# Performance work log

Hardware: AMD Instinct MI355X
Metric: run time of the kernel (lower is better)

## Reference

```python
import jax, jax.numpy as jnp
import numpy as np
from jax.ops import segment_sum, segment_max

N = 50000
E = 800000
F_IN = 128
F_HEAD = 32
HEADS = 8
N_CLASSES = 32
NEG_SLOPE = 0.2


def setup_inputs() -> dict:
    key = jax.random.key(0)
    ks = jax.random.split(key, 12)
    x = jax.random.normal(ks[0], (N, F_IN), dtype=jnp.float32)
    edge_index = jax.random.randint(ks[1], (2, E), 0, N, dtype=jnp.int64)
    # layer 1 params (in=128 -> heads=8, out=32)
    s1 = 1.0 / np.sqrt(F_IN)
    W1 = jax.random.uniform(ks[2], (F_IN, HEADS * F_HEAD), jnp.float32, -s1, s1)
    a_src1 = jax.random.uniform(ks[3], (HEADS, F_HEAD), jnp.float32, -s1, s1)
    a_dst1 = jax.random.uniform(ks[4], (HEADS, F_HEAD), jnp.float32, -s1, s1)
    b1 = jnp.zeros((HEADS * F_HEAD,), jnp.float32)
    # layer 2 params (in=256 -> heads=1, out=32)
    s2 = 1.0 / np.sqrt(HEADS * F_HEAD)
    W2 = jax.random.uniform(ks[5], (HEADS * F_HEAD, N_CLASSES), jnp.float32, -s2, s2)
    a_src2 = jax.random.uniform(ks[6], (1, N_CLASSES), jnp.float32, -s2, s2)
    a_dst2 = jax.random.uniform(ks[7], (1, N_CLASSES), jnp.float32, -s2, s2)
    b2 = jnp.zeros((N_CLASSES,), jnp.float32)
    return {"x": x, "edge_index": edge_index, "W1": W1, "a_src1": a_src1,
            "a_dst1": a_dst1, "b1": b1, "W2": W2, "a_src2": a_src2,
            "a_dst2": a_dst2, "b2": b2}


def gat_conv(x, W, a_src, a_dst, b, src, dst, heads, out_ch):
    n = x.shape[0]
    h = (x @ W).reshape(n, heads, out_ch)                  # [N,H,F]
    alpha_src = jnp.einsum('nhf,hf->nh', h, a_src)         # [N,H]
    alpha_dst = jnp.einsum('nhf,hf->nh', h, a_dst)
    e = alpha_src[src] + alpha_dst[dst]                    # [E,H]
    e = jnp.where(e > 0, e, NEG_SLOPE * e)                 # LeakyReLU(0.2)
    # segment softmax over edges grouped by destination node
    m = segment_max(e, dst, num_segments=n)                # [N,H]
    ex = jnp.exp(e - m[dst])
    denom = segment_sum(ex, dst, num_segments=n)           # [N,H]
    alpha = ex / (denom[dst] + 1e-16)                      # [E,H]
    out = segment_sum(alpha[:, :, None] * h[src], dst, num_segments=n)  # [N,H,F]
    return out.reshape(n, heads * out_ch) + b


def reference(x, edge_index, W1, a_src1, a_dst1, b1, W2, a_src2, a_dst2, b2):
    src, dst = edge_index[0], edge_index[1]
    h = gat_conv(x, W1, a_src1, a_dst1, b1, src, dst, HEADS, F_HEAD)
    h = jax.nn.elu(h)
    out = gat_conv(h, W2, a_src2, a_dst2, b2, src, dst, 1, N_CLASSES)
    return out
```

## Files before the change

kernel.cpp:

```cpp
#include <hip/hip_runtime.h>
#include <math.h>

#define NNODES 50000
#define NEDGES 800000
#define GB 782

typedef _Float16 f16;
typedef _Float16 f16x8 __attribute__((ext_vector_type(8)));
typedef _Float16 f16x4 __attribute__((ext_vector_type(4)));
typedef _Float16 f16x2 __attribute__((ext_vector_type(2)));
typedef float f32x4 __attribute__((ext_vector_type(4)));
typedef float f32x8 __attribute__((ext_vector_type(8)));
typedef unsigned short u16;


__global__ __launch_bounds__(256) void k_deg_wfrag(const int* __restrict__ ei, int* __restrict__ deg,
                                                   int* __restrict__ rank,
                                                   const float* __restrict__ W1, const float* __restrict__ W2,
                                                   f16* __restrict__ W1f, f16* __restrict__ W2f) {
    int bid = blockIdx.x;
    if (bid < NEDGES / 256) {
        int e = bid * 256 + threadIdx.x;
        rank[e] = atomicAdd(&deg[ei[NEDGES + e]], 1);
    } else {
        int id = (bid - NEDGES / 256) * 256 + threadIdx.x;
        if (id < 32768) {
            int k = id >> 8, c = id & 255;
            int kc = k >> 5, quad = (k & 31) >> 3, j = k & 7;
            W1f[(((kc << 8) + c) * 4 + quad) * 8 + j] = (f16)W1[id];
        } else {
            int i2 = id - 32768;
            int k = i2 >> 5, c = i2 & 31;
            int kc = k >> 5, quad = (k & 31) >> 3, j = k & 7;
            W2f[(((kc << 5) + c) * 4 + quad) * 8 + j] = (f16)W2[i2];
        }
    }
}

__global__ __launch_bounds__(256) void k_scanA(const int* __restrict__ deg, int* __restrict__ incl,
                                               int* __restrict__ partial) {
    int t = threadIdx.x;
    int i = blockIdx.x * 256 + t;
    int v = (i < NNODES) ? deg[i] : 0;
    int lane = t & 63, wid = t >> 6;
    int s = v;
#pragma unroll
    for (int d = 1; d < 64; d <<= 1) { int u = __shfl_up(s, d, 64); if (lane >= d) s += u; }
    __shared__ int wtot[4];
    if (lane == 63) wtot[wid] = s;
    __syncthreads();
    int off = 0;
    for (int w = 0; w < wid; ++w) off += wtot[w];
    s += off;
    if (i < NNODES) incl[i] = s;
    if (t == 255) partial[blockIdx.x] = s;
}

__global__ __launch_bounds__(256) void k_scanC(const int* __restrict__ deg, const int* __restrict__ incl,
                                               const int* __restrict__ partial, int* __restrict__ rowst) {
    int t = threadIdx.x, bid = blockIdx.x;
    int v = (t < bid) ? partial[t] : 0;
    int lane = t & 63, wid = t >> 6;
#pragma unroll
    for (int d = 1; d < 64; d <<= 1) v += __shfl_xor(v, d);
    __shared__ int ws[4];
    if (lane == 0) ws[wid] = v;
    __syncthreads();
    int choff = ws[0] + ws[1] + ws[2] + ws[3];
    int i = bid * 256 + t;
    if (i < NNODES) {
        int rs1 = incl[i] + choff;
        rowst[i + 1] = rs1;
        if (i == 0) rowst[0] = 0;
    }
}


__global__ __launch_bounds__(256) void k_gemm1_sc(const float* __restrict__ X, const f16* __restrict__ W1f,
                                                  const float* __restrict__ Asrc, const float* __restrict__ Adst,
                                                  f16* __restrict__ h1s, float* __restrict__ as1,
                                                  float* __restrict__ ad1, const int* __restrict__ ei,
                                                  const int* __restrict__ rowst, const int* __restrict__ rank,
                                                  u16* __restrict__ sd16) {
    __shared__ f16 sA[64 * 136];
    int bid = blockIdx.x;
    int t = threadIdx.x;
    if (bid >= GB) {
        int e = (bid - GB) * 256 + t;
        if (e < NEDGES) {
            int s = ei[e], d = ei[NEDGES + e];
            int pos = rowst[d] + rank[e];
            sd16[pos] = (u16)s;
        }
        return;
    }
    int bm = bid * 64;
    int lane = t & 63, w = t >> 6;
    int r = lane & 15, quad = lane >> 4;
    int cw = w * 64;
    f16x8 bf[4][4];
#pragma unroll
    for (int kc = 0; kc < 4; ++kc)
#pragma unroll
        for (int nt = 0; nt < 4; ++nt)
            bf[kc][nt] = *(const f16x8*)&W1f[(((kc << 8) + cw + nt * 16 + r) * 4 + quad) * 8];
#pragma unroll
    for (int i = 0; i < 8; ++i) {
        int idx = i * 256 + t;
        int row = idx >> 5, c4 = (idx & 31) << 2;
        int gr = bm + row;
        float4 v = make_float4(0.f, 0.f, 0.f, 0.f);
        if (gr < NNODES) v = *(const float4*)(X + (size_t)gr * 128 + c4);
        f16x4 h = {(f16)v.x, (f16)v.y, (f16)v.z, (f16)v.w};
        *(f16x4*)&sA[row * 136 + c4] = h;
    }
    __syncthreads();
    f32x4 acc[4][4];
#pragma unroll
    for (int rg = 0; rg < 4; ++rg)
#pragma unroll
        for (int nt = 0; nt < 4; ++nt) acc[rg][nt] = (f32x4){0.f, 0.f, 0.f, 0.f};
#pragma unroll
    for (int kc = 0; kc < 4; ++kc)
#pragma unroll
        for (int rg = 0; rg < 4; ++rg) {
            f16x8 a = *(f16x8*)&sA[(rg * 16 + r) * 136 + kc * 32 + quad * 8];
#pragma unroll
            for (int nt = 0; nt < 4; ++nt)
                acc[rg][nt] = __builtin_amdgcn_mfma_f32_16x16x32_f16(a, bf[kc][nt], acc[rg][nt], 0, 0, 0);
        }
#pragma unroll
    for (int rg = 0; rg < 4; ++rg)
#pragma unroll
        for (int nt = 0; nt < 4; ++nt)
#pragma unroll
            for (int i = 0; i < 4; ++i) {
                int gr = bm + rg * 16 + quad * 4 + i;
                if (gr < NNODES)
                    h1s[((size_t)(2 * w + (nt >> 1)) * NNODES + gr) * 32 + (nt & 1) * 16 + r] =
                        (f16)acc[rg][nt][i];
            }
    float asv[4], adv[4];
#pragma unroll
    for (int nt = 0; nt < 4; ++nt) {
        asv[nt] = Asrc[cw + nt * 16 + r];
        adv[nt] = Adst[cw + nt * 16 + r];
    }
#pragma unroll
    for (int rg = 0; rg < 4; ++rg)
#pragma unroll
        for (int i = 0; i < 4; ++i) {
            int gr = bm + rg * 16 + quad * 4 + i;
#pragma unroll
            for (int hh = 0; hh < 2; ++hh) {
                float ps = acc[rg][2 * hh][i] * asv[2 * hh] + acc[rg][2 * hh + 1][i] * asv[2 * hh + 1];
                float pd = acc[rg][2 * hh][i] * adv[2 * hh] + acc[rg][2 * hh + 1][i] * adv[2 * hh + 1];
#pragma unroll
                for (int off = 1; off < 16; off <<= 1) {
                    ps += __shfl_xor(ps, off);
                    pd += __shfl_xor(pd, off);
                }
                if (r == 0 && gr < NNODES) {
                    as1[(size_t)(2 * w + hh) * NNODES + gr] = ps;
                    ad1[(size_t)(2 * w + hh) * NNODES + gr] = pd;
                }
            }
        }
}

__global__ __launch_bounds__(256) void k_gemm2(const f16* __restrict__ h2s, const f16* __restrict__ W2f,
                                               const float* __restrict__ Asrc, const float* __restrict__ Adst,
                                               f16* __restrict__ gh, float* __restrict__ as2,
                                               float* __restrict__ ad2) {
    int t = threadIdx.x;
    int bm = blockIdx.x * 64;
    int lane = t & 63, w = t >> 6;
    int r = lane & 15, quad = lane >> 4;
    int r0 = w * 16;
    int gra = bm + r0 + r;
    int grac = gra < NNODES ? gra : 0;
    f32x4 acc[2];
    acc[0] = (f32x4){0.f, 0.f, 0.f, 0.f};
    acc[1] = (f32x4){0.f, 0.f, 0.f, 0.f};
#pragma unroll
    for (int kc = 0; kc < 8; ++kc) {
        f16x8 a = *(const f16x8*)(h2s + ((size_t)kc * NNODES + grac) * 32 + quad * 8);
#pragma unroll
        for (int nt = 0; nt < 2; ++nt) {
            f16x8 b = *(const f16x8*)&W2f[(((kc << 5) + nt * 16 + r) * 4 + quad) * 8];
            acc[nt] = __builtin_amdgcn_mfma_f32_16x16x32_f16(a, b, acc[nt], 0, 0, 0);
        }
    }
#pragma unroll
    for (int nt = 0; nt < 2; ++nt)
#pragma unroll
        for (int i = 0; i < 4; ++i) {
            int gr = bm + r0 + quad * 4 + i;
            if (gr < NNODES) gh[(size_t)gr * 32 + nt * 16 + r] = (f16)acc[nt][i];
        }
    float as0 = Asrc[r], as16 = Asrc[16 + r];
    float ad0 = Adst[r], ad16 = Adst[16 + r];
#pragma unroll
    for (int i = 0; i < 4; ++i) {
        int gr = bm + r0 + quad * 4 + i;
        float ps = acc[0][i] * as0 + acc[1][i] * as16;
        float pd = acc[0][i] * ad0 + acc[1][i] * ad16;
#pragma unroll
        for (int off = 1; off < 16; off <<= 1) {
            ps += __shfl_xor(ps, off);
            pd += __shfl_xor(pd, off);
        }
        if (r == 0 && gr < NNODES) { as2[gr] = ps; ad2[gr] = pd; }
    }
}

__global__ __launch_bounds__(256) void k_agg1(const int* __restrict__ rowst, const u16* __restrict__ sd16,
                                              const float* __restrict__ as1, const float* __restrict__ ad1,
                                              const f16* __restrict__ h1s, const float* __restrict__ b1,
                                              f16* __restrict__ h2s) {
    int bid = blockIdx.x;
    int sl = bid & 7;
    int ng = bid >> 3;
    int t = threadIdx.x;
    int w = t >> 6, lane = t & 63;
    int g = lane >> 2, cs = lane & 3;
    int c0 = cs << 3;
    int n = ng * 64 + w * 16 + g;
    if (n >= NNODES) return;
    int s = rowst[n], e = rowst[n + 1];
    float adn = ad1[(size_t)sl * NNODES + n];
    const f16* __restrict__ hp = h1s + (size_t)sl * NNODES * 32 + c0;
    const float* __restrict__ ap = as1 + (size_t)sl * NNODES;
    f32x8 acc = (f32x8){0.f, 0.f, 0.f, 0.f, 0.f, 0.f, 0.f, 0.f};
    float sum = 0.f;
    int j = s;
    for (; j + 7 < e; j += 8) {
        int si[8];
#pragma unroll
        for (int u = 0; u < 8; ++u) si[u] = (int)sd16[j + u];
        float xv[8];
#pragma unroll
        for (int u = 0; u < 8; ++u) xv[u] = ap[si[u]];
        f16x8 vv[8];
#pragma unroll
        for (int u = 0; u < 8; ++u) vv[u] = *(const f16x8*)(hp + (size_t)si[u] * 32);
        float ee[8];
#pragma unroll
        for (int u = 0; u < 8; ++u) {
            float x = xv[u] + adn;
            x = fmaxf(x, 0.2f * x);
            ee[u] = __expf(x);
            sum += ee[u];
        }
#pragma unroll
        for (int k = 0; k < 8; ++k) {
            float a = acc[k];
#pragma unroll
            for (int u = 0; u < 8; ++u) a += ee[u] * (float)vv[u][k];
            acc[k] = a;
        }
    }
    for (; j + 3 < e; j += 4) {
        int si[4];
#pragma unroll
        for (int u = 0; u < 4; ++u) si[u] = (int)sd16[j + u];
        float xv[4];
#pragma unroll
        for (int u = 0; u < 4; ++u) xv[u] = ap[si[u]];
        f16x8 vv[4];
#pragma unroll
        for (int u = 0; u < 4; ++u) vv[u] = *(const f16x8*)(hp + (size_t)si[u] * 32);
        float ee[4];
#pragma unroll
        for (int u = 0; u < 4; ++u) {
            float x = xv[u] + adn;
            x = fmaxf(x, 0.2f * x);
            ee[u] = __expf(x);
            sum += ee[u];
        }
#pragma unroll
        for (int k = 0; k < 8; ++k) {
            float a = acc[k];
#pragma unroll
            for (int u = 0; u < 4; ++u) a += ee[u] * (float)vv[u][k];
            acc[k] = a;
        }
    }
    for (; j < e; ++j) {
        int s0 = (int)sd16[j];
        float x0 = ap[s0] + adn;
        f16x8 v0 = *(const f16x8*)(hp + (size_t)s0 * 32);
        x0 = fmaxf(x0, 0.2f * x0);
        float e0 = __expf(x0);
        sum += e0;
#pragma unroll
        for (int k = 0; k < 8; ++k) acc[k] += e0 * (float)v0[k];
    }
    float inv = 1.f / (sum + 1e-16f);
    float4 b0 = *(const float4*)(b1 + sl * 32 + c0);
    float4 b4 = *(const float4*)(b1 + sl * 32 + c0 + 4);
    float o[8] = {acc[0] * inv + b0.x, acc[1] * inv + b0.y, acc[2] * inv + b0.z, acc[3] * inv + b0.w,
                  acc[4] * inv + b4.x, acc[5] * inv + b4.y, acc[6] * inv + b4.z, acc[7] * inv + b4.w};
    f16x8 oh;
#pragma unroll
    for (int k = 0; k < 8; ++k) {
        float v = o[k];
        v = v > 0.f ? v : __expf(v) - 1.f;
        oh[k] = (f16)v;
    }
    *(f16x8*)(h2s + ((size_t)sl * NNODES + n) * 32 + c0) = oh;
}

__global__ __launch_bounds__(256) void k_agg2(const int* __restrict__ rowst, const u16* __restrict__ sd16,
                                              const float* __restrict__ as2, const float* __restrict__ ad2,
                                              const f16* __restrict__ gh, const float* __restrict__ b2,
                                              float* __restrict__ out) {
    int w = threadIdx.x >> 6, lane = threadIdx.x & 63;
    int n = blockIdx.x * 4 + w;
    int s = rowst[n], e = rowst[n + 1];
    int slot = lane >> 4;
    int cp = lane & 15;
    float adn = ad2[n];
    const f16* __restrict__ gp = gh + 2 * cp;
    float a0 = 0.f, a1 = 0.f, sum = 0.f;
    int j = s + slot;
    for (; j + 12 < e; j += 16) {
        int si[4];
#pragma unroll
        for (int u = 0; u < 4; ++u) si[u] = (int)sd16[j + 4 * u];
        float xv[4];
#pragma unroll
        for (int u = 0; u < 4; ++u) xv[u] = as2[si[u]];
        f16x2 vv[4];
#pragma unroll
        for (int u = 0; u < 4; ++u) vv[u] = *(const f16x2*)(gp + (size_t)si[u] * 32);
        float ee[4];
#pragma unroll
        for (int u = 0; u < 4; ++u) {
            float x = xv[u] + adn;
            x = fmaxf(x, 0.2f * x);
            ee[u] = __expf(x);
            sum += ee[u];
        }
#pragma unroll
        for (int u = 0; u < 4; ++u) a0 += ee[u] * (float)vv[u][0];
#pragma unroll
        for (int u = 0; u < 4; ++u) a1 += ee[u] * (float)vv[u][1];
    }
    for (; j + 4 < e; j += 8) {
        int s0 = (int)sd16[j];
        int s1 = (int)sd16[j + 4];
        float x0 = as2[s0] + adn, x1 = as2[s1] + adn;
        f16x2 v0 = *(const f16x2*)(gp + (size_t)s0 * 32);
        f16x2 v1 = *(const f16x2*)(gp + (size_t)s1 * 32);
        x0 = fmaxf(x0, 0.2f * x0);
        x1 = fmaxf(x1, 0.2f * x1);
        float e0 = __expf(x0), e1 = __expf(x1);
        sum += e0 + e1;
        a0 += e0 * (float)v0[0] + e1 * (float)v1[0];
        a1 += e0 * (float)v0[1] + e1 * (float)v1[1];
    }
    for (; j < e; j += 4) {
        int s0 = (int)sd16[j];
        float x0 = as2[s0] + adn;
        f16x2 v0 = *(const f16x2*)(gp + (size_t)s0 * 32);
        x0 = fmaxf(x0, 0.2f * x0);
        float e0 = __expf(x0);
        sum += e0;
        a0 += e0 * (float)v0[0];
        a1 += e0 * (float)v0[1];
    }
#pragma unroll
    for (int d = 16; d < 64; d <<= 1) {
        sum += __shfl_xor(sum, d);
        a0 += __shfl_xor(a0, d);
        a1 += __shfl_xor(a1, d);
    }
    if (slot == 0) {
        float inv = 1.f / (sum + 1e-16f);
        float2 o;
        o.x = a0 * inv + b2[2 * cp];
        o.y = a1 * inv + b2[2 * cp + 1];
        *(float2*)(out + (size_t)n * 32 + 2 * cp) = o;
    }
}


extern "C" void kernel_launch(void* const* d_in, const int* in_sizes, int n_in,
                              void* d_out, int out_size, void* d_ws, size_t ws_size,
                              hipStream_t stream) {
    const float* x    = (const float*)d_in[0];
    const int*   ei   = (const int*)d_in[1];
    const float* W1   = (const float*)d_in[2];
    const float* As1  = (const float*)d_in[3];
    const float* Ad1  = (const float*)d_in[4];
    const float* b1   = (const float*)d_in[5];
    const float* W2   = (const float*)d_in[6];
    const float* As2  = (const float*)d_in[7];
    const float* Ad2  = (const float*)d_in[8];
    const float* b2   = (const float*)d_in[9];
    float* out = (float*)d_out;

    char* p = (char*)d_ws;
    auto alloc = [&](size_t bytes) -> char* {
        char* r = p;
        p += (bytes + 255) & ~(size_t)255;
        return r;
    };
    f16* h1s      = (f16*)alloc((size_t)NNODES * 256 * 2);
    f16* h2s      = (f16*)alloc((size_t)NNODES * 256 * 2);
    f16* W1f      = (f16*)alloc((size_t)128 * 256 * 2);
    f16* W2f      = (f16*)alloc((size_t)256 * 32 * 2);
    f16* gh       = (f16*)alloc((size_t)NNODES * 32 * 2);
    float* asrc1  = (float*)alloc((size_t)NNODES * 8 * 4);
    float* adst1  = (float*)alloc((size_t)NNODES * 8 * 4);
    float* asrc2  = (float*)alloc((size_t)NNODES * 4);
    float* adst2  = (float*)alloc((size_t)NNODES * 4);
    int* deg      = (int*)alloc((size_t)NNODES * 4);
    int* incl     = (int*)alloc((size_t)NNODES * 4);
    int* rowst    = (int*)alloc((size_t)(NNODES + 1) * 4);
    int* rank     = (int*)alloc((size_t)NEDGES * 4);
    u16* sdc      = (u16*)alloc((size_t)NEDGES * 2);
    int* partial  = (int*)alloc(256 * 4);

    const int EB = NEDGES / 256;
    const int NCH = (NNODES + 255) / 256;

    hipMemsetAsync(deg, 0, (size_t)NNODES * 4, stream);
    k_deg_wfrag<<<EB + 160, 256, 0, stream>>>(ei, deg, rank, W1, W2, W1f, W2f);
    k_scanA<<<NCH, 256, 0, stream>>>(deg, incl, partial);
    k_scanC<<<NCH, 256, 0, stream>>>(deg, incl, partial, rowst);

    k_gemm1_sc<<<GB + EB, 256, 0, stream>>>(x, W1f, As1, Ad1, h1s, asrc1, adst1, ei, rowst, rank, sdc);
    k_agg1<<<8 * GB, 256, 0, stream>>>(rowst, sdc, asrc1, adst1, h1s, b1, h2s);

    k_gemm2<<<(NNODES + 63) / 64, 256, 0, stream>>>(h2s, W2f, As2, Ad2, gh, asrc2, adst2);
    k_agg2<<<NNODES / 4, 256, 0, stream>>>(rowst, sdc, asrc2, adst2, gh, b2, out);
}
```

Baseline: 252.1 us.

## Precompute per-edge attention exponentials in a separate pass with padded CSR rows

Each CSR row is padded to a multiple of 8, and every entry now stores a packed (dst,src) pair. A new edge-parallel kernel computes exp(LeakyReLU(a_src+a_dst)) for all 8 heads once per edge and writes them head-major, with padding entries set to zero. k_agg1 then streams these weights with vector loads and runs a single unrolled loop with no remainder loops. This replaces the eight separate gathers of a_src and the repeated exp work across head-slices with about 38 MB of extra write and read traffic, an extra memset and an extra kernel launch.

```diff
diff --git a/kernel.cpp b/kernel.cpp
--- a/kernel.cpp
+++ b/kernel.cpp
@@ -4,6 +4,7 @@
 #define NNODES 50000
 #define NEDGES 800000
 #define GB 782
+#define EPB 1200000
 
 typedef _Float16 f16;
 typedef _Float16 f16x8 __attribute__((ext_vector_type(8)));
@@ -41,7 +42,7 @@
                                                int* __restrict__ partial) {
     int t = threadIdx.x;
     int i = blockIdx.x * 256 + t;
-    int v = (i < NNODES) ? deg[i] : 0;
+    int v = (i < NNODES) ? ((deg[i] + 7) & ~7) : 0;
     int lane = t & 63, wid = t >> 6;
     int s = v;
 #pragma unroll
@@ -78,10 +79,10 @@
 
 __global__ __launch_bounds__(256) void k_gemm1_sc(const float* __restrict__ X, const f16* __restrict__ W1f,
                                                   const float* __restrict__ Asrc, const float* __restrict__ Adst,
-                                                  f16* __restrict__ h1s, float* __restrict__ as1,
-                                                  float* __restrict__ ad1, const int* __restrict__ ei,
+                                                  f16* __restrict__ h1s, float* __restrict__ as1n,
+                                                  float* __restrict__ ad1n, const int* __restrict__ ei,
                                                   const int* __restrict__ rowst, const int* __restrict__ rank,
-                                                  u16* __restrict__ sd16) {
+                                                  unsigned* __restrict__ sd32) {
     __shared__ f16 sA[64 * 136];
     int bid = blockIdx.x;
     int t = threadIdx.x;
@@ -90,7 +91,7 @@
         if (e < NEDGES) {
             int s = ei[e], d = ei[NEDGES + e];
             int pos = rowst[d] + rank[e];
-            sd16[pos] = (u16)s;
+            sd32[pos] = ((unsigned)d << 16) | (unsigned)s;
         }
         return;
     }
@@ -161,11 +162,38 @@
                     pd += __shfl_xor(pd, off);
                 }
                 if (r == 0 && gr < NNODES) {
-                    as1[(size_t)(2 * w + hh) * NNODES + gr] = ps;
-                    ad1[(size_t)(2 * w + hh) * NNODES + gr] = pd;
+                    as1n[(size_t)gr * 8 + 2 * w + hh] = ps;
+                    ad1n[(size_t)gr * 8 + 2 * w + hh] = pd;
                 }
             }
         }
+}
+
+__global__ __launch_bounds__(256) void k_exp(unsigned* __restrict__ sd32, const float* __restrict__ as1n,
+                                             const float* __restrict__ ad1n, float* __restrict__ exph) {
+    int j = blockIdx.x * 256 + threadIdx.x;
+    if (j >= EPB) return;
+    unsigned q = sd32[j];
+    int d = (int)(q >> 16);
+    if (d >= NNODES) {
+        sd32[j] = 0u;
+#pragma unroll
+        for (int h = 0; h < 8; ++h) exph[(size_t)h * EPB + j] = 0.f;
+        return;
+    }
+    int s = (int)(q & 0xffffu);
+    float4 a0 = *(const float4*)(as1n + (size_t)s * 8);
+    float4 a1 = *(const float4*)(as1n + (size_t)s * 8 + 4);
+    float4 d0 = *(const float4*)(ad1n + (size_t)d * 8);
+    float4 d1 = *(const float4*)(ad1n + (size_t)d * 8 + 4);
+    float av[8] = {a0.x, a0.y, a0.z, a0.w, a1.x, a1.y, a1.z, a1.w};
+    float dv[8] = {d0.x, d0.y, d0.z, d0.w, d1.x, d1.y, d1.z, d1.w};
+#pragma unroll
+    for (int h = 0; h < 8; ++h) {
+        float x = av[h] + dv[h];
+        x = fmaxf(x, 0.2f * x);
+        exph[(size_t)h * EPB + j] = __expf(x);
+    }
 }
 
 __global__ __launch_bounds__(256) void k_gemm2(const f16* __restrict__ h2s, const f16* __restrict__ W2f,
@@ -214,10 +242,9 @@
     }
 }
 
-__global__ __launch_bounds__(256) void k_agg1(const int* __restrict__ rowst, const u16* __restrict__ sd16,
-                                              const float* __restrict__ as1, const float* __restrict__ ad1,
-                                              const f16* __restrict__ h1s, const float* __restrict__ b1,
-                                              f16* __restrict__ h2s) {
+__global__ __launch_bounds__(256) void k_agg1(const int* __restrict__ rowst, const unsigned* __restrict__ sd32,
+                                              const float* __restrict__ exph, const f16* __restrict__ h1s,
+                                              const float* __restrict__ b1, f16* __restrict__ h2s) {
     int bid = blockIdx.x;
     int sl = bid & 7;
     int ng = bid >> 3;
@@ -228,30 +255,22 @@
     int n = ng * 64 + w * 16 + g;
     if (n >= NNODES) return;
     int s = rowst[n], e = rowst[n + 1];
-    float adn = ad1[(size_t)sl * NNODES + n];
     const f16* __restrict__ hp = h1s + (size_t)sl * NNODES * 32 + c0;
-    const float* __restrict__ ap = as1 + (size_t)sl * NNODES;
+    const float* __restrict__ ep = exph + (size_t)sl * EPB;
     f32x8 acc = (f32x8){0.f, 0.f, 0.f, 0.f, 0.f, 0.f, 0.f, 0.f};
     float sum = 0.f;
-    int j = s;
-    for (; j + 7 < e; j += 8) {
-        int si[8];
-#pragma unroll
-        for (int u = 0; u < 8; ++u) si[u] = (int)sd16[j + u];
-        float xv[8];
-#pragma unroll
-        for (int u = 0; u < 8; ++u) xv[u] = ap[si[u]];
+    for (int j = s; j < e; j += 8) {
+        uint4 q0 = *(const uint4*)(sd32 + j);
+        uint4 q1 = *(const uint4*)(sd32 + j + 4);
+        float4 e0 = *(const float4*)(ep + j);
+        float4 e1 = *(const float4*)(ep + j + 4);
+        int si[8] = {(int)(q0.x & 0xffffu), (int)(q0.y & 0xffffu), (int)(q0.z & 0xffffu), (int)(q0.w & 0xffffu),
+                     (int)(q1.x & 0xffffu), (int)(q1.y & 0xffffu), (int)(q1.z & 0xffffu), (int)(q1.w & 0xffffu)};
         f16x8 vv[8];
 #pragma unroll
         for (int u = 0; u < 8; ++u) vv[u] = *(const f16x8*)(hp + (size_t)si[u] * 32);
-        float ee[8];
-#pragma unroll
-        for (int u = 0; u < 8; ++u) {
-            float x = xv[u] + adn;
-            x = fmaxf(x, 0.2f * x);
-            ee[u] = __expf(x);
-            sum += ee[u];
-        }
+        float ee[8] = {e0.x, e0.y, e0.z, e0.w, e1.x, e1.y, e1.z, e1.w};
+        sum += ((e0.x + e0.y) + (e0.z + e0.w)) + ((e1.x + e1.y) + (e1.z + e1.w));
 #pragma unroll
         for (int k = 0; k < 8; ++k) {
             float a = acc[k];
@@ -259,42 +278,6 @@
             for (int u = 0; u < 8; ++u) a += ee[u] * (float)vv[u][k];
             acc[k] = a;
         }
-    }
-    for (; j + 3 < e; j += 4) {
-        int si[4];
-#pragma unroll
-        for (int u = 0; u < 4; ++u) si[u] = (int)sd16[j + u];
-        float xv[4];
-#pragma unroll
-        for (int u = 0; u < 4; ++u) xv[u] = ap[si[u]];
-        f16x8 vv[4];
-#pragma unroll
-        for (int u = 0; u < 4; ++u) vv[u] = *(const f16x8*)(hp + (size_t)si[u] * 32);
-        float ee[4];
-#pragma unroll
-        for (int u = 0; u < 4; ++u) {
-            float x = xv[u] + adn;
-            x = fmaxf(x, 0.2f * x);
-            ee[u] = __expf(x);
-            sum += ee[u];
-        }
-#pragma unroll
-        for (int k = 0; k < 8; ++k) {
-            float a = acc[k];
-#pragma unroll
-            for (int u = 0; u < 4; ++u) a += ee[u] * (float)vv[u][k];
-            acc[k] = a;
-        }
-    }
-    for (; j < e; ++j) {
-        int s0 = (int)sd16[j];
-        float x0 = ap[s0] + adn;
-        f16x8 v0 = *(const f16x8*)(hp + (size_t)s0 * 32);
-        x0 = fmaxf(x0, 0.2f * x0);
-        float e0 = __expf(x0);
-        sum += e0;
-#pragma unroll
-        for (int k = 0; k < 8; ++k) acc[k] += e0 * (float)v0[k];
     }
     float inv = 1.f / (sum + 1e-16f);
     float4 b0 = *(const float4*)(b1 + sl * 32 + c0);
@@ -311,13 +294,14 @@
     *(f16x8*)(h2s + ((size_t)sl * NNODES + n) * 32 + c0) = oh;
 }
 
-__global__ __launch_bounds__(256) void k_agg2(const int* __restrict__ rowst, const u16* __restrict__ sd16,
+__global__ __launch_bounds__(256) void k_agg2(const int* __restrict__ rowst, const unsigned* __restrict__ sd32,
+                                              const int* __restrict__ deg,
                                               const float* __restrict__ as2, const float* __restrict__ ad2,
                                               const f16* __restrict__ gh, const float* __restrict__ b2,
                                               float* __restrict__ out) {
     int w = threadIdx.x >> 6, lane = threadIdx.x & 63;
     int n = blockIdx.x * 4 + w;
-    int s = rowst[n], e = rowst[n + 1];
+    int s = rowst[n], e = s + deg[n];
     int slot = lane >> 4;
     int cp = lane & 15;
     float adn = ad2[n];
@@ -327,7 +311,7 @@
     for (; j + 12 < e; j += 16) {
         int si[4];
 #pragma unroll
-        for (int u = 0; u < 4; ++u) si[u] = (int)sd16[j + 4 * u];
+        for (int u = 0; u < 4; ++u) si[u] = (int)(sd32[j + 4 * u] & 0xffffu);
         float xv[4];
 #pragma unroll
         for (int u = 0; u < 4; ++u) xv[u] = as2[si[u]];
@@ -348,8 +332,8 @@
         for (int u = 0; u < 4; ++u) a1 += ee[u] * (float)vv[u][1];
     }
     for (; j + 4 < e; j += 8) {
-        int s0 = (int)sd16[j];
-        int s1 = (int)sd16[j + 4];
+        int s0 = (int)(sd32[j] & 0xffffu);
+        int s1 = (int)(sd32[j + 4] & 0xffffu);
         float x0 = as2[s0] + adn, x1 = as2[s1] + adn;
         f16x2 v0 = *(const f16x2*)(gp + (size_t)s0 * 32);
         f16x2 v1 = *(const f16x2*)(gp + (size_t)s1 * 32);
@@ -361,7 +345,7 @@
         a1 += e0 * (float)v0[1] + e1 * (float)v1[1];
     }
     for (; j < e; j += 4) {
-        int s0 = (int)sd16[j];
+        int s0 = (int)(sd32[j] & 0xffffu);
         float x0 = as2[s0] + adn;
         f16x2 v0 = *(const f16x2*)(gp + (size_t)s0 * 32);
         x0 = fmaxf(x0, 0.2f * x0);
@@ -412,28 +396,32 @@
     f16* W1f      = (f16*)alloc((size_t)128 * 256 * 2);
     f16* W2f      = (f16*)alloc((size_t)256 * 32 * 2);
     f16* gh       = (f16*)alloc((size_t)NNODES * 32 * 2);
-    float* asrc1  = (float*)alloc((size_t)NNODES * 8 * 4);
-    float* adst1  = (float*)alloc((size_t)NNODES * 8 * 4);
+    float* as1n   = (float*)alloc((size_t)NNODES * 8 * 4);
+    float* ad1n   = (float*)alloc((size_t)NNODES * 8 * 4);
     float* asrc2  = (float*)alloc((size_t)NNODES * 4);
     float* adst2  = (float*)alloc((size_t)NNODES * 4);
     int* deg      = (int*)alloc((size_t)NNODES * 4);
     int* incl     = (int*)alloc((size_t)NNODES * 4);
     int* rowst    = (int*)alloc((size_t)(NNODES + 1) * 4);
     int* rank     = (int*)alloc((size_t)NEDGES * 4);
-    u16* sdc      = (u16*)alloc((size_t)NEDGES * 2);
+    unsigned* sdc = (unsigned*)alloc((size_t)EPB * 4);
+    float* exph   = (float*)alloc((size_t)8 * EPB * 4);
     int* partial  = (int*)alloc(256 * 4);
 
     const int EB = NEDGES / 256;
     const int NCH = (NNODES + 255) / 256;
+    const int XB = (EPB + 255) / 256;
 
     hipMemsetAsync(deg, 0, (size_t)NNODES * 4, stream);
+    hipMemsetAsync(sdc, 0xFF, (size_t)EPB * 4, stream);
     k_deg_wfrag<<<EB + 160, 256, 0, stream>>>(ei, deg, rank, W1, W2, W1f, W2f);
     k_scanA<<<NCH, 256, 0, stream>>>(deg, incl, partial);
     k_scanC<<<NCH, 256, 0, stream>>>(deg, incl, partial, rowst);
 
-    k_gemm1_sc<<<GB + EB, 256, 0, stream>>>(x, W1f, As1, Ad1, h1s, asrc1, adst1, ei, rowst, rank, sdc);
-    k_agg1<<<8 * GB, 256, 0, stream>>>(rowst, sdc, asrc1, adst1, h1s, b1, h2s);
+    k_gemm1_sc<<<GB + EB, 256, 0, stream>>>(x, W1f, As1, Ad1, h1s, as1n, ad1n, ei, rowst, rank, sdc);
+    k_exp<<<XB, 256, 0, stream>>>(sdc, as1n, ad1n, exph);
+    k_agg1<<<8 * GB, 256, 0, stream>>>(rowst, sdc, exph, h1s, b1, h2s);
 
     k_gemm2<<<(NNODES + 63) / 64, 256, 0, stream>>>(h2s, W2f, As2, Ad2, gh, asrc2, adst2);
-    k_agg2<<<NNODES / 4, 256, 0, stream>>>(rowst, sdc, asrc2, adst2, gh, b2, out);
-}
+    k_agg2<<<NNODES / 4, 256, 0, stream>>>(rowst, sdc, deg, asrc2, adst2, gh, b2, out);
+}
```

Result: slower. 265.2 us (+5.2%).
